# Kernel tuning notes

Measured on AMD Instinct MI355X. Metric: run time of the kernel, lower is better.

## Reference

```python
import jax, jax.numpy as jnp
import numpy as np

NEG_SLOPE = 0.2  # PyG GATConv default


def gat_conv(x, src, dst, W, a_src, a_dst, bias, n):
    # x: [N, Fin] -> h: [N, Fout]
    h = x @ W
    alpha_s = h @ a_src  # [N]
    alpha_d = h @ a_dst  # [N]
    e = jax.nn.leaky_relu(alpha_s[src] + alpha_d[dst], NEG_SLOPE)  # [E]
    # segment softmax over incoming edges of each target node
    m = jax.ops.segment_max(e, dst, num_segments=n)
    e = jnp.exp(e - m[dst])
    denom = jax.ops.segment_sum(e, dst, num_segments=n)
    alpha = e / denom[dst]
    out = jax.ops.segment_sum(alpha[:, None] * h[src], dst, num_segments=n)
    return out + bias


def setup_inputs() -> dict:
    key = jax.random.key(0)
    ks = jax.random.split(key, 10)
    N, E, FIN, HID, FOUT = 100000, 3200000, 128, 32, 64
    x = jax.random.normal(ks[0], (N, FIN), dtype=jnp.float32)
    edge_index = jax.random.randint(ks[1], (2, E), 0, N, dtype=jnp.int64)
    s = 1.0 / np.sqrt(FIN)
    W1 = jax.random.normal(ks[2], (FIN, HID), dtype=jnp.float32) * s
    a1_src = jax.random.normal(ks[3], (HID,), dtype=jnp.float32) * 0.1
    a1_dst = jax.random.normal(ks[4], (HID,), dtype=jnp.float32) * 0.1
    b1 = jnp.zeros((HID,), dtype=jnp.float32)
    W2 = jax.random.normal(ks[5], (HID, FOUT), dtype=jnp.float32) * (1.0 / np.sqrt(HID))
    a2_src = jax.random.normal(ks[6], (FOUT,), dtype=jnp.float32) * 0.1
    a2_dst = jax.random.normal(ks[7], (FOUT,), dtype=jnp.float32) * 0.1
    b2 = jnp.zeros((FOUT,), dtype=jnp.float32)
    return {"x": x, "edge_index": edge_index, "W1": W1, "a1_src": a1_src,
            "a1_dst": a1_dst, "b1": b1, "W2": W2, "a2_src": a2_src,
            "a2_dst": a2_dst, "b2": b2}


def reference(x, edge_index, W1, a1_src, a1_dst, b1, W2, a2_src, a2_dst, b2):
    n = x.shape[0]
    # add self loops (GATConv default add_self_loops=True)
    loop = jnp.arange(n, dtype=edge_index.dtype)
    src = jnp.concatenate([edge_index[0], loop])
    dst = jnp.concatenate([edge_index[1], loop])
    h = gat_conv(x, src, dst, W1, a1_src, a1_dst, b1, n)
    h = jax.nn.relu(h)
    out = gat_conv(h, src, dst, W2, a2_src, a2_dst, b2, n)
    return out
```

## Files before the change

### kernel.cpp

```cpp
#include <hip/hip_runtime.h>
#include <cstdint>
#include <cmath>

#define NEG_SLOPE 0.2f
#define BSH 6
#define BR  64
#define CSH 11
#define EBUF_CAP 8192
#define PCHUNK 8192

__device__ __forceinline__ float leaky(float v) { return v > 0.f ? v : NEG_SLOPE * v; }
__device__ __forceinline__ float uf(unsigned u) { return __uint_as_float(u); }

__device__ __forceinline__ unsigned short f2bf(float f) {
    unsigned u = __float_as_uint(f);
    unsigned r = ((u >> 16) & 1u) + 0x7fffu;
    return (unsigned short)((u + r) >> 16);
}
__device__ __forceinline__ float bflo(unsigned q) { return __uint_as_float(q << 16); }
__device__ __forceinline__ float bfhi(unsigned q) { return __uint_as_float(q & 0xffff0000u); }

template <int FIN, int FOUT, int CPR, int LCPR>
__global__ __launch_bounds__(256, 4) void gemm_rows(
    const float* __restrict__ X, const float* __restrict__ W,
    const float* __restrict__ a_src, const float* __restrict__ a_dst,
    unsigned short* __restrict__ H, float* __restrict__ As, float* __restrict__ Ad,
    int N)
{
    constexpr int ROWS = 256 / CPR;
    constexpr int XST = FIN + 4;
    static_assert((1 << LCPR) == CPR && CPR * 4 == FOUT, "geometry");

    __shared__ float Ws[FIN * FOUT];
    __shared__ float Xs[ROWS * XST];

    const int tid = threadIdx.x;
    const int base = blockIdx.x * ROWS;

    for (int i = tid; i < FIN * FOUT / 4; i += 256)
        reinterpret_cast<float4*>(Ws)[i] = reinterpret_cast<const float4*>(W)[i];

    for (int i = tid; i < ROWS * FIN / 4; i += 256) {
        int row = i / (FIN / 4);
        int k4 = (i - row * (FIN / 4)) * 4;
        float4 v = make_float4(0.f, 0.f, 0.f, 0.f);
        if (base + row < N)
            v = *reinterpret_cast<const float4*>(&X[(size_t)(base + row) * FIN + k4]);
        *reinterpret_cast<float4*>(&Xs[row * XST + k4]) = v;
    }
    __syncthreads();

    const int colg = tid & (CPR - 1);
    const int row = tid >> LCPR;
    const int c0 = colg * 4;

    float4 acc = make_float4(0.f, 0.f, 0.f, 0.f);

#pragma unroll 2
    for (int k = 0; k < FIN; k += 4) {
        float4 xv = *reinterpret_cast<const float4*>(&Xs[row * XST + k]);
        float4 w0 = *reinterpret_cast<const float4*>(&Ws[(k + 0) * FOUT + c0]);
        float4 w1 = *reinterpret_cast<const float4*>(&Ws[(k + 1) * FOUT + c0]);
        float4 w2 = *reinterpret_cast<const float4*>(&Ws[(k + 2) * FOUT + c0]);
        float4 w3 = *reinterpret_cast<const float4*>(&Ws[(k + 3) * FOUT + c0]);
        acc.x = fmaf(xv.w, w3.x, fmaf(xv.z, w2.x, fmaf(xv.y, w1.x, fmaf(xv.x, w0.x, acc.x))));
        acc.y = fmaf(xv.w, w3.y, fmaf(xv.z, w2.y, fmaf(xv.y, w1.y, fmaf(xv.x, w0.y, acc.y))));
        acc.z = fmaf(xv.w, w3.z, fmaf(xv.z, w2.z, fmaf(xv.y, w1.z, fmaf(xv.x, w0.z, acc.z))));
        acc.w = fmaf(xv.w, w3.w, fmaf(xv.z, w2.w, fmaf(xv.y, w1.w, fmaf(xv.x, w0.w, acc.w))));
    }

    const int grow = base + row;
    if (grow < N) {
        ushort4 hv;
        hv.x = f2bf(acc.x); hv.y = f2bf(acc.y);
        hv.z = f2bf(acc.z); hv.w = f2bf(acc.w);
        *reinterpret_cast<ushort4*>(&H[(size_t)grow * FOUT + c0]) = hv;
    }

    float4 asv = *reinterpret_cast<const float4*>(&a_src[c0]);
    float4 adv = *reinterpret_cast<const float4*>(&a_dst[c0]);
    float ps = acc.x * asv.x + acc.y * asv.y + acc.z * asv.z + acc.w * asv.w;
    float pd = acc.x * adv.x + acc.y * adv.y + acc.z * adv.z + acc.w * adv.w;
#pragma unroll
    for (int ofs = 1; ofs < CPR; ofs <<= 1) {
        ps += __shfl_xor(ps, ofs);
        pd += __shfl_xor(pd, ofs);
    }
    if (colg == 0 && grow < N) { As[grow] = ps; Ad[grow] = pd; }
}

__global__ __launch_bounds__(256) void bucket_hist(
    const int* __restrict__ dst, int* __restrict__ bhist, int E, int NB)
{
    __shared__ int hc[2048];
    for (int i = threadIdx.x; i < 2048; i += 256) hc[i] = 0;
    __syncthreads();
    for (int e = blockIdx.x * 256 + threadIdx.x; e < E; e += gridDim.x * 256)
        atomicAdd(&hc[dst[e] >> BSH], 1);
    __syncthreads();
    for (int i = threadIdx.x; i < NB; i += 256)
        if (hc[i]) atomicAdd(&bhist[i], hc[i]);
}

__global__ __launch_bounds__(256) void bucket_scan(
    const int* __restrict__ bhist, int* __restrict__ boff,
    int* __restrict__ ftail, int* __restrict__ ctail, int NB, int NC)
{
    __shared__ int sd[256];
    const int t = threadIdx.x;
    const int CH = (NB + 255) >> 8;
    int s = 0;
    for (int j = 0; j < CH; ++j) {
        int idx = t * CH + j;
        s += (idx < NB) ? bhist[idx] : 0;
    }
    sd[t] = s; __syncthreads();
    for (int ofs = 1; ofs < 256; ofs <<= 1) {
        int tmp = (t >= ofs) ? sd[t - ofs] : 0;
        __syncthreads();
        sd[t] += tmp;
        __syncthreads();
    }
    int run = sd[t] - s;
    for (int j = 0; j < CH; ++j) {
        int idx = t * CH + j;
        if (idx < NB) {
            boff[idx] = run;
            ftail[idx * 16] = run;
            run += bhist[idx];
        }
    }
    if (t == 255) boff[NB] = run;
    __syncthreads();
    if (t < NC) {
        int f0 = t << 5;
        ctail[t * 16] = boff[f0 < NB ? f0 : NB];
    }
}

__global__ __launch_bounds__(256) void coarse_partition(
    const int* __restrict__ src, const int* __restrict__ dst,
    int* __restrict__ ctail, int* __restrict__ csrA, int E, int NC)
{
    __shared__ int lhist[64], lcur[64], gpos[64];
    const int t = threadIdx.x;
    if (t < 64) { lhist[t] = 0; lcur[t] = 0; }
    __syncthreads();
    const int base = blockIdx.x * PCHUNK;
    int bb[32], pp[32];
#pragma unroll
    for (int i = 0; i < 32; ++i) {
        int e = base + i * 256 + t;
        bb[i] = -1;
        if (e < E) {
            int sv = src[e], dv = dst[e];
            bb[i] = dv >> CSH;
            pp[i] = (sv << CSH) | (dv & ((1 << CSH) - 1));
            atomicAdd(&lhist[bb[i]], 1);
        }
    }
    __syncthreads();
    if (t < NC && lhist[t]) gpos[t] = atomicAdd(&ctail[t * 16], lhist[t]);
    __syncthreads();
#pragma unroll
    for (int i = 0; i < 32; ++i) {
        if (bb[i] >= 0) {
            int b = bb[i];
            csrA[gpos[b] + atomicAdd(&lcur[b], 1)] = pp[i];
        }
    }
}

__global__ __launch_bounds__(256) void fine_partition(
    const int* __restrict__ csrA, const int* __restrict__ boff,
    int* __restrict__ ftail, int* __restrict__ csrB, int NB)
{
    __shared__ int lhist[32], lcur[32], gpos[32];
    const int b = blockIdx.x;
    const int t = threadIdx.x;
    const int f0 = b << 5;
    const int fe = (f0 + 32 < NB) ? f0 + 32 : NB;
    const int cstart = boff[f0 < NB ? f0 : NB];
    const int cend = boff[fe];
    const int start = cstart + blockIdx.y * PCHUNK;
    if (start >= cend) return;
    const int end = (start + PCHUNK < cend) ? start + PCHUNK : cend;
    if (t < 32) { lhist[t] = 0; lcur[t] = 0; }
    __syncthreads();
    int ff[32], pp[32];
#pragma unroll
    for (int i = 0; i < 32; ++i) {
        int e = start + i * 256 + t;
        ff[i] = -1;
        if (e < end) {
            int v = csrA[e];
            int sv = v >> CSH, dl = v & ((1 << CSH) - 1);
            ff[i] = dl >> BSH;
            pp[i] = (sv << BSH) | (dl & (BR - 1));
            atomicAdd(&lhist[ff[i]], 1);
        }
    }
    __syncthreads();
    if (t < 32 && lhist[t]) gpos[t] = atomicAdd(&ftail[(f0 + t) * 16], lhist[t]);
    __syncthreads();
#pragma unroll
    for (int i = 0; i < 32; ++i) {
        if (ff[i] >= 0) {
            int f = ff[i];
            csrB[gpos[f] + atomicAdd(&lcur[f], 1)] = pp[i];
        }
    }
}

__global__ __launch_bounds__(256) void bucket_build(
    int* __restrict__ csr, const int* __restrict__ boff,
    int* __restrict__ off, int N, int NB)
{
    __shared__ int ebuf[EBUF_CAP];
    __shared__ int lcnt[BR];
    __shared__ int lpref[BR];
    const int bi = blockIdx.x;
    const int t = threadIdx.x;
    const int nb0 = bi << BSH;
    const int p0 = boff[bi];
    const int p1 = boff[bi + 1];
    const int cnt = p1 - p0;

    if (t < BR) lcnt[t] = 0;
    __syncthreads();
    for (int i = t; i < cnt; i += 256) {
        int v = csr[p0 + i];
        if (i < EBUF_CAP) ebuf[i] = v;
        atomicAdd(&lcnt[v & (BR - 1)], 1);
    }
    __syncthreads();
    if (t < BR) {
        int c = lcnt[t];
        int sc = c;
#pragma unroll
        for (int ofs = 1; ofs < BR; ofs <<= 1) {
            int o = __shfl_up(sc, ofs);
            if (t >= ofs) sc += o;
        }
        lpref[t] = sc - c;
        int n = nb0 + t;
        if (n < N) off[n] = p0 + sc - c;
        lcnt[t] = 0;
    }
    if (bi == NB - 1 && t == 0) off[N] = p1;
    __syncthreads();
    for (int i = t; i < cnt && i < EBUF_CAP; i += 256) {
        int v = ebuf[i];
        int ln = v & (BR - 1);
        int p = atomicAdd(&lcnt[ln], 1);
        csr[p0 + lpref[ln] + p] = v >> BSH;
    }
}

template <int F, bool RELU>
__global__ __launch_bounds__(256) void gat_aggregate(
    const int* __restrict__ csr, const int* __restrict__ off,
    const float* __restrict__ As, const float* __restrict__ Ad,
    const unsigned short* __restrict__ Hb, const float* __restrict__ bias,
    float* __restrict__ Out, int N)
{
    constexpr int LPR = F / 2;
    constexpr int EPI = 64 / LPR;
    constexpr unsigned RB = F * 2;

    __shared__ uint2 pr[4][64];
    const int wave = threadIdx.x >> 6;
    const int lane = threadIdx.x & 63;
    const int n = blockIdx.x * 4 + wave;
    if (n >= N) return;

    const int o0 = off[n];
    const int deg = off[n + 1] - o0;
    const float adn = Ad[n];
    const float eself = leaky(As[n] + adn);

    float m = eself;
    for (int i = lane; i < deg; i += 64) {
        int s = csr[o0 + i];
        m = fmaxf(m, leaky(As[s] + adn));
    }
#pragma unroll
    for (int ofs = 32; ofs; ofs >>= 1) m = fmaxf(m, __shfl_xor(m, ofs));

    uint2* myp = pr[wave];
    const char* Hc = (const char*)Hb;
    const int sub = lane / LPR;
    const unsigned f4 = (unsigned)(lane & (LPR - 1)) * 4u;

    float2 acc = make_float2(0.f, 0.f);
    float denp = 0.f;

    for (int c = 0; c < deg; c += 64) {
        int i = c + lane;
        float w = 0.f; unsigned sb = 0;
        if (i < deg) {
            int s = csr[o0 + i];
            w = __expf(leaky(As[s] + adn) - m);
            sb = (unsigned)s * RB;
            denp += w;
        }
        myp[lane] = make_uint2(sb, __float_as_uint(w));
        int lim = (deg - c < 64) ? deg - c : 64;
        int j = sub;
        for (; j + 3 * EPI < lim; j += 4 * EPI) {
            uint2 p0 = myp[j], p1 = myp[j + EPI], p2 = myp[j + 2 * EPI], p3 = myp[j + 3 * EPI];
            unsigned q0 = *(const unsigned*)(Hc + p0.x + f4);
            unsigned q1 = *(const unsigned*)(Hc + p1.x + f4);
            unsigned q2 = *(const unsigned*)(Hc + p2.x + f4);
            unsigned q3 = *(const unsigned*)(Hc + p3.x + f4);
            float w0 = uf(p0.y), w1 = uf(p1.y), w2 = uf(p2.y), w3 = uf(p3.y);
            acc.x = fmaf(w0, bflo(q0), acc.x); acc.y = fmaf(w0, bfhi(q0), acc.y);
            acc.x = fmaf(w1, bflo(q1), acc.x); acc.y = fmaf(w1, bfhi(q1), acc.y);
            acc.x = fmaf(w2, bflo(q2), acc.x); acc.y = fmaf(w2, bfhi(q2), acc.y);
            acc.x = fmaf(w3, bflo(q3), acc.x); acc.y = fmaf(w3, bfhi(q3), acc.y);
        }
        for (; j < lim; j += EPI) {
            uint2 p = myp[j];
            unsigned q = *(const unsigned*)(Hc + p.x + f4);
            float w0 = uf(p.y);
            acc.x = fmaf(w0, bflo(q), acc.x);
            acc.y = fmaf(w0, bfhi(q), acc.y);
        }
    }

#pragma unroll
    for (int ofs = 32; ofs >= LPR; ofs >>= 1) {
        acc.x += __shfl_xor(acc.x, ofs);
        acc.y += __shfl_xor(acc.y, ofs);
    }
#pragma unroll
    for (int ofs = 1; ofs < 64; ofs <<= 1) denp += __shfl_xor(denp, ofs);

    float wsf = __expf(eself - m);
    unsigned qs = *(const unsigned*)(Hc + (size_t)n * RB + f4);
    acc.x = fmaf(wsf, bflo(qs), acc.x);
    acc.y = fmaf(wsf, bfhi(qs), acc.y);
    float den = denp + wsf;

    if (sub == 0) {
        int fi = (lane & (LPR - 1)) * 2;
        float vx = acc.x / den + bias[fi];
        float vy = acc.y / den + bias[fi + 1];
        if (RELU) { vx = fmaxf(vx, 0.f); vy = fmaxf(vy, 0.f); }
        *reinterpret_cast<float2*>(&Out[(size_t)n * F + fi]) = make_float2(vx, vy);
    }
}

extern "C" void kernel_launch(void* const* d_in, const int* in_sizes, int n_in,
                              void* d_out, int out_size, void* d_ws, size_t ws_size,
                              hipStream_t stream)
{
    const float* x   = (const float*)d_in[0];
    const int*   ei  = (const int*)d_in[1];
    const float* W1  = (const float*)d_in[2];
    const float* a1s = (const float*)d_in[3];
    const float* a1d = (const float*)d_in[4];
    const float* b1  = (const float*)d_in[5];
    const float* W2  = (const float*)d_in[6];
    const float* a2s = (const float*)d_in[7];
    const float* a2d = (const float*)d_in[8];
    const float* b2  = (const float*)d_in[9];

    const int N = in_sizes[0] / 128;
    const int E = in_sizes[1] / 2;
    const int NB = (N + BR - 1) >> BSH;
    const int NC = (N + (1 << CSH) - 1) >> CSH;
    const int* src = ei;
    const int* dst = ei + E;
    float* out = (float*)d_out;

    float* ws = (float*)d_ws;
    size_t o = 0;
    unsigned short* h1b = (unsigned short*)(ws + o); o += (size_t)N * 16;
    float* h1a = ws + o; o += (size_t)N * 32;
    unsigned short* h2b = (unsigned short*)(ws + o); o += (size_t)N * 32;
    float* as1 = ws + o; o += N;
    float* ad1 = ws + o; o += N;
    float* as2 = ws + o; o += N;
    float* ad2 = ws + o; o += N;
    int* ip = (int*)(ws + o);
    size_t io = 0;
    int* bhist = ip + io; io += NB;
    int* boff  = ip + io; io += (NB + 1);
    int* ftail = ip + io; io += (size_t)NB * 16;
    int* ctail = ip + io; io += (size_t)NC * 16;
    int* off   = ip + io; io += (N + 1);
    int* csrA  = ip + io; io += E;
    int* csrB  = ip + io; io += E;

    hipMemsetAsync(bhist, 0, (size_t)NB * sizeof(int), stream);

    bucket_hist<<<256, 256, 0, stream>>>(dst, bhist, E, NB);
    bucket_scan<<<1, 256, 0, stream>>>(bhist, boff, ftail, ctail, NB, NC);
    coarse_partition<<<(E + PCHUNK - 1) / PCHUNK, 256, 0, stream>>>(
        src, dst, ctail, csrA, E, NC);
    fine_partition<<<dim3(NC, 9), 256, 0, stream>>>(csrA, boff, ftail, csrB, NB);
    bucket_build<<<NB, 256, 0, stream>>>(csrB, boff, off, N, NB);

    const int gn = (N + 3) / 4;

    gemm_rows<128, 32, 8, 3><<<(N + 31) / 32, 256, 0, stream>>>(
        x, W1, a1s, a1d, h1b, as1, ad1, N);
    gat_aggregate<32, true><<<gn, 256, 0, stream>>>(
        csrB, off, as1, ad1, h1b, b1, h1a, N);

    gemm_rows<32, 64, 16, 4><<<(N + 15) / 16, 256, 0, stream>>>(
        h1a, W2, a2s, a2d, h2b, as2, ad2, N);
    gat_aggregate<64, false><<<gn, 256, 0, stream>>>(
        csrB, off, as2, ad2, h2b, b2, out, N);
}
```

Measured before the change: 286.6 us.

## Replace per-node softmax max pass with global As upper bound; widen feature loads

Instead of a separate pass over each node's incoming edges to compute the segment max, the GEMM kernel now reduces a global maximum of alpha_src via an ordered-int atomicMax. The aggregate kernel uses leaky(gmax + Ad[n]) as the softmax shift, which is a valid upper bound because leaky_relu is monotone. This removes one gather sweep over csr and As per node. Separately, each lane now handles 4 bf16 features with 8-byte loads instead of 2, halving lanes per row. The risk is exp underflow when the global bound sits far above a node's true maximum, and the new code leaves a stray unused 'sub' expression.

New measurement: 666.1 us. 132% more time.

```diff
diff --git a/kernel.cpp b/kernel.cpp
--- a/kernel.cpp
+++ b/kernel.cpp
@@ -12,6 +12,14 @@
 __device__ __forceinline__ float leaky(float v) { return v > 0.f ? v : NEG_SLOPE * v; }
 __device__ __forceinline__ float uf(unsigned u) { return __uint_as_float(u); }
 
+__device__ __forceinline__ unsigned f2ord(float f) {
+    unsigned b = __float_as_uint(f);
+    return (b & 0x80000000u) ? ~b : (b | 0x80000000u);
+}
+__device__ __forceinline__ float ord2f(unsigned u) {
+    return (u & 0x80000000u) ? __uint_as_float(u ^ 0x80000000u) : __uint_as_float(~u);
+}
+
 __device__ __forceinline__ unsigned short f2bf(float f) {
     unsigned u = __float_as_uint(f);
     unsigned r = ((u >> 16) & 1u) + 0x7fffu;
@@ -25,7 +33,7 @@
     const float* __restrict__ X, const float* __restrict__ W,
     const float* __restrict__ a_src, const float* __restrict__ a_dst,
     unsigned short* __restrict__ H, float* __restrict__ As, float* __restrict__ Ad,
-    int N)
+    unsigned* __restrict__ gmax, int N)
 {
     constexpr int ROWS = 256 / CPR;
     constexpr int XST = FIN + 4;
@@ -87,6 +95,11 @@
         pd += __shfl_xor(pd, ofs);
     }
     if (colg == 0 && grow < N) { As[grow] = ps; Ad[grow] = pd; }
+
+    float pm = (grow < N) ? ps : -3.0e38f;
+#pragma unroll
+    for (int ofs = 1; ofs < 64; ofs <<= 1) pm = fmaxf(pm, __shfl_xor(pm, ofs));
+    if ((tid & 63) == 0) atomicMax(gmax, f2ord(pm));
 }
 
 __global__ __launch_bounds__(256) void bucket_hist(
@@ -262,9 +275,9 @@
     const int* __restrict__ csr, const int* __restrict__ off,
     const float* __restrict__ As, const float* __restrict__ Ad,
     const unsigned short* __restrict__ Hb, const float* __restrict__ bias,
-    float* __restrict__ Out, int N)
-{
-    constexpr int LPR = F / 2;
+    const unsigned* __restrict__ gmax, float* __restrict__ Out, int N)
+{
+    constexpr int LPR = F / 4;
     constexpr int EPI = 64 / LPR;
     constexpr unsigned RB = F * 2;
 
@@ -278,21 +291,15 @@
     const int deg = off[n + 1] - o0;
     const float adn = Ad[n];
     const float eself = leaky(As[n] + adn);
-
-    float m = eself;
-    for (int i = lane; i < deg; i += 64) {
-        int s = csr[o0 + i];
-        m = fmaxf(m, leaky(As[s] + adn));
-    }
-#pragma unroll
-    for (int ofs = 32; ofs; ofs >>= 1) m = fmaxf(m, __shfl_xor(m, ofs));
+    const float m = leaky(ord2f(*gmax) + adn);
 
     uint2* myp = pr[wave];
     const char* Hc = (const char*)Hb;
-    const int sub = lane / LPR;
-    const unsigned f4 = (unsigned)(lane & (LPR - 1)) * 4u;
-
-    float2 acc = make_float2(0.f, 0.f);
+    const int sub = lane >> (6 - __builtin_ctz(EPI) == 0 ? 6 : 0), dummy = 0; (void)dummy;
+    const int subg = lane / LPR;
+    const unsigned f8 = (unsigned)(lane & (LPR - 1)) * 8u;
+
+    float4 acc = make_float4(0.f, 0.f, 0.f, 0.f);
     float denp = 0.f;
 
     for (int c = 0; c < deg; c += 64) {
@@ -306,25 +313,29 @@
         }
         myp[lane] = make_uint2(sb, __float_as_uint(w));
         int lim = (deg - c < 64) ? deg - c : 64;
-        int j = sub;
+        int j = subg;
         for (; j + 3 * EPI < lim; j += 4 * EPI) {
             uint2 p0 = myp[j], p1 = myp[j + EPI], p2 = myp[j + 2 * EPI], p3 = myp[j + 3 * EPI];
-            unsigned q0 = *(const unsigned*)(Hc + p0.x + f4);
-            unsigned q1 = *(const unsigned*)(Hc + p1.x + f4);
-            unsigned q2 = *(const unsigned*)(Hc + p2.x + f4);
-            unsigned q3 = *(const unsigned*)(Hc + p3.x + f4);
+            uint2 q0 = *(const uint2*)(Hc + p0.x + f8);
+            uint2 q1 = *(const uint2*)(Hc + p1.x + f8);
+            uint2 q2 = *(const uint2*)(Hc + p2.x + f8);
+            uint2 q3 = *(const uint2*)(Hc + p3.x + f8);
             float w0 = uf(p0.y), w1 = uf(p1.y), w2 = uf(p2.y), w3 = uf(p3.y);
-            acc.x = fmaf(w0, bflo(q0), acc.x); acc.y = fmaf(w0, bfhi(q0), acc.y);
-            acc.x = fmaf(w1, bflo(q1), acc.x); acc.y = fmaf(w1, bfhi(q1), acc.y);
-            acc.x = fmaf(w2, bflo(q2), acc.x); acc.y = fmaf(w2, bfhi(q2), acc.y);
-            acc.x = fmaf(w3, bflo(q3), acc.x); acc.y = fmaf(w3, bfhi(q3), acc.y);
+            acc.x = fmaf(w0, bflo(q0.x), acc.x); acc.y = fmaf(w0, bfhi(q0.x), acc.y);
+            acc.z = fmaf(w0, bflo(q0.y), acc.z); acc.w = fmaf(w0, bfhi(q0.y), acc.w);
+            acc.x = fmaf(w1, bflo(q1.x), acc.x); acc.y = fmaf(w1, bfhi(q1.x), acc.y);
+            acc.z = fmaf(w1, bflo(q1.y), acc.z); acc.w = fmaf(w1, bfhi(q1.y), acc.w);
+            acc.x = fmaf(w2, bflo(q2.x), acc.x); acc.y = fmaf(w2, bfhi(q2.x), acc.y);
+            acc.z = fmaf(w2, bflo(q2.y), acc.z); acc.w = fmaf(w2, bfhi(q2.y), acc.w);
+            acc.x = fmaf(w3, bflo(q3.x), acc.x); acc.y = fmaf(w3, bfhi(q3.x), acc.y);
+            acc.z = fmaf(w3, bflo(q3.y), acc.z); acc.w = fmaf(w3, bfhi(q3.y), acc.w);
         }
         for (; j < lim; j += EPI) {
             uint2 p = myp[j];
-            unsigned q = *(const unsigned*)(Hc + p.x + f4);
+            uint2 q = *(const uint2*)(Hc + p.x + f8);
             float w0 = uf(p.y);
-            acc.x = fmaf(w0, bflo(q), acc.x);
-            acc.y = fmaf(w0, bfhi(q), acc.y);
+            acc.x = fmaf(w0, bflo(q.x), acc.x); acc.y = fmaf(w0, bfhi(q.x), acc.y);
+            acc.z = fmaf(w0, bflo(q.y), acc.z); acc.w = fmaf(w0, bfhi(q.y), acc.w);
         }
     }
 
@@ -332,22 +343,31 @@
     for (int ofs = 32; ofs >= LPR; ofs >>= 1) {
         acc.x += __shfl_xor(acc.x, ofs);
         acc.y += __shfl_xor(acc.y, ofs);
+        acc.z += __shfl_xor(acc.z, ofs);
+        acc.w += __shfl_xor(acc.w, ofs);
     }
 #pragma unroll
     for (int ofs = 1; ofs < 64; ofs <<= 1) denp += __shfl_xor(denp, ofs);
 
     float wsf = __expf(eself - m);
-    unsigned qs = *(const unsigned*)(Hc + (size_t)n * RB + f4);
-    acc.x = fmaf(wsf, bflo(qs), acc.x);
-    acc.y = fmaf(wsf, bfhi(qs), acc.y);
+    uint2 qs = *(const uint2*)(Hc + (size_t)n * RB + f8);
+    acc.x = fmaf(wsf, bflo(qs.x), acc.x); acc.y = fmaf(wsf, bfhi(qs.x), acc.y);
+    acc.z = fmaf(wsf, bflo(qs.y), acc.z); acc.w = fmaf(wsf, bfhi(qs.y), acc.w);
     float den = denp + wsf;
 
-    if (sub == 0) {
-        int fi = (lane & (LPR - 1)) * 2;
-        float vx = acc.x / den + bias[fi];
-        float vy = acc.y / den + bias[fi + 1];
-        if (RELU) { vx = fmaxf(vx, 0.f); vy = fmaxf(vy, 0.f); }
-        *reinterpret_cast<float2*>(&Out[(size_t)n * F + fi]) = make_float2(vx, vy);
+    if (subg == 0) {
+        int fi = (lane & (LPR - 1)) * 4;
+        float4 bv = *reinterpret_cast<const float4*>(&bias[fi]);
+        float4 v;
+        v.x = acc.x / den + bv.x;
+        v.y = acc.y / den + bv.y;
+        v.z = acc.z / den + bv.z;
+        v.w = acc.w / den + bv.w;
+        if (RELU) {
+            v.x = fmaxf(v.x, 0.f); v.y = fmaxf(v.y, 0.f);
+            v.z = fmaxf(v.z, 0.f); v.w = fmaxf(v.w, 0.f);
+        }
+        *reinterpret_cast<float4*>(&Out[(size_t)n * F + fi]) = v;
     }
 }
 
@@ -385,6 +405,8 @@
     float* ad2 = ws + o; o += N;
     int* ip = (int*)(ws + o);
     size_t io = 0;
+    unsigned* gmax1 = (unsigned*)(ip + io); io += 1;
+    unsigned* gmax2 = (unsigned*)(ip + io); io += 1;
     int* bhist = ip + io; io += NB;
     int* boff  = ip + io; io += (NB + 1);
     int* ftail = ip + io; io += (size_t)NB * 16;
@@ -393,7 +415,7 @@
     int* csrA  = ip + io; io += E;
     int* csrB  = ip + io; io += E;
 
-    hipMemsetAsync(bhist, 0, (size_t)NB * sizeof(int), stream);
+    hipMemsetAsync(ip, 0, (size_t)(NB + 2) * sizeof(int), stream);
 
     bucket_hist<<<256, 256, 0, stream>>>(dst, bhist, E, NB);
     bucket_scan<<<1, 256, 0, stream>>>(bhist, boff, ftail, ctail, NB, NC);
@@ -405,12 +427,12 @@
     const int gn = (N + 3) / 4;
 
     gemm_rows<128, 32, 8, 3><<<(N + 31) / 32, 256, 0, stream>>>(
-        x, W1, a1s, a1d, h1b, as1, ad1, N);
+        x, W1, a1s, a1d, h1b, as1, ad1, gmax1, N);
     gat_aggregate<32, true><<<gn, 256, 0, stream>>>(
-        csrB, off, as1, ad1, h1b, b1, h1a, N);
+        csrB, off, as1, ad1, h1b, b1, gmax1, h1a, N);
 
     gemm_rows<32, 64, 16, 4><<<(N + 15) / 16, 256, 0, stream>>>(
-        h1a, W2, a2s, a2d, h2b, as2, ad2, N);
+        h1a, W2, a2s, a2d, h2b, as2, ad2, gmax2, N);
     gat_aggregate<64, false><<<gn, 256, 0, stream>>>(
-        csrB, off, as2, ad2, h2b, b2, out, N);
-}
+        csrB, off, as2, ad2, h2b, b2, gmax2, out, N);
+}
```
